# Kernel optimization log

Hardware: AMD Instinct MI355X
Metric: run time of the kernel (lower is better)

## Reference

```python
import jax, jax.numpy as jnp
import numpy as np

B, C, S = 16, 8, 128
DT, DX, DY = 0.001, 1.0, 1.0
NUM_STEPS = 10
EPS = 1e-6


def _thomas(a, b, c, d):
    """Batched Thomas tridiagonal solve. a,b,c,d: [M,N] rows; solve along N."""
    aT, bT, cT, dT = a.T, b.T, c.T, d.T  # [N, M]
    zero = jnp.zeros_like(dT[0])

    def fwd(carry, inp):
        cs_p, ds_p = carry
        ai, bi, ci, di = inp
        denom = bi - ai * cs_p + EPS  # i=0: cs_p=0 -> denom = b0 + eps (matches torch)
        cs = ci / denom
        ds = (di - ai * ds_p) / denom
        return (cs, ds), (cs, ds)

    _, (c_star, d_star) = jax.lax.scan(fwd, (zero, zero), (aT, bT, cT, dT))

    def bwd(x_next, inp):
        ci, di = inp
        x = di - ci * x_next
        return x, x

    _, xs = jax.lax.scan(bwd, d_star[-1], (c_star[:-1], d_star[:-1]), reverse=True)
    x = jnp.concatenate([xs, d_star[-1:]], axis=0)  # [N, M]
    return x.T


def _diffuse_rows(u2d, coeff):
    """Implicit 1D diffusion along last axis. u2d, coeff: [M,N]."""
    a = -coeff
    c = -coeff
    b = 1.0 + 2.0 * coeff
    b = b.at[:, 0].set(1.0 + coeff[:, 0])
    b = b.at[:, -1].set(1.0 + coeff[:, -1])
    return _thomas(a, b, c, u2d)


def _forward(u, alpha_base, beta_base, alpha_time_coeff, beta_time_coeff, channel_mixing):
    Bb, Cc, H, W = u.shape
    half = DT / 2.0
    t = 0.0
    for _ in range(NUM_STEPS):
        # x half-step (coefficient alpha at time t)
        alpha = jnp.clip(alpha_base + alpha_time_coeff * t, EPS, 10.0)
        u = jnp.einsum('dc,bchw->bdhw', channel_mixing, u)
        uf = u.reshape(Bb * Cc, H, W)
        af = jnp.broadcast_to(alpha[None], (Bb, Cc, H, W)).reshape(Bb * Cc, H, W)
        uf = _diffuse_rows(uf.reshape(-1, W), af.reshape(-1, W) * half / DX**2).reshape(Bb * Cc, H, W)
        t += half
        # y full step (coefficient beta at time t+dt/2)
        beta = jnp.clip(beta_base + beta_time_coeff * t, EPS, 10.0)
        bf = jnp.broadcast_to(beta[None], (Bb, Cc, H, W)).reshape(Bb * Cc, H, W)
        ut = uf.transpose(0, 2, 1).reshape(-1, H)
        bt = bf.transpose(0, 2, 1).reshape(-1, H)
        ut = _diffuse_rows(ut, bt * DT / DY**2)
        uf = ut.reshape(Bb * Cc, W, H).transpose(0, 2, 1)
        t += half
        # x half-step (coefficient alpha at time t+dt)
        alpha = jnp.clip(alpha_base + alpha_time_coeff * t, EPS, 10.0)
        af = jnp.broadcast_to(alpha[None], (Bb, Cc, H, W)).reshape(Bb * Cc, H, W)
        uf = _diffuse_rows(uf.reshape(-1, W), af.reshape(-1, W) * half / DX**2).reshape(Bb * Cc, H, W)
        u = uf.reshape(Bb, Cc, H, W)
    return u


def setup_inputs() -> dict:
    key = jax.random.key(0)
    k_u, k_cm, k_atc, k_btc = jax.random.split(key, 4)
    u = jax.random.normal(k_u, (B, C, S, S), dtype=jnp.float32)
    alpha_base = jnp.ones((C, S, S), dtype=jnp.float32)
    beta_base = jnp.ones((C, S, S), dtype=jnp.float32)
    alpha_time_coeff = jax.random.normal(k_atc, (C, S, S), dtype=jnp.float32) * 0.01
    beta_time_coeff = jax.random.normal(k_btc, (C, S, S), dtype=jnp.float32) * 0.01
    channel_mixing = jnp.eye(C, dtype=jnp.float32) + jax.random.normal(k_cm, (C, C), dtype=jnp.float32) * 0.01
    return {
        'u': u,
        'alpha_base': alpha_base,
        'beta_base': beta_base,
        'alpha_time_coeff': alpha_time_coeff,
        'beta_time_coeff': beta_time_coeff,
        'channel_mixing': channel_mixing,
    }


def reference(u, alpha_base, beta_base, alpha_time_coeff, beta_time_coeff, channel_mixing):
    return _forward(u, alpha_base, beta_base, alpha_time_coeff, beta_time_coeff, channel_mixing)
```

## Files before the change

### kernel.cpp

```cpp
#include <hip/hip_runtime.h>


constexpr int S_ = 128;
constexpr int RS = 129;
constexpr float EPSF = 1e-6f;

constexpr int OFF_X  = 0;
constexpr int OFF_C  = 32 * RS;
constexpr int OFF_B  = 64 * RS;
constexpr int OFF_HA = 96 * RS;

template <int N>
__device__ __forceinline__ void jrunN(const float (&e)[N], const float (&g)[N],
                                      float (&o)[N - 4]) {
    float x1[N];
    #pragma unroll
    for (int i = 1; i <= N - 2; ++i) x1[i] = fmaf(g[i], e[i - 1] + e[i + 1], e[i]);
    #pragma unroll
    for (int i = 2; i <= N - 3; ++i) o[i - 2] = fmaf(g[i], x1[i - 1] + x1[i + 1], e[i]);
}

template <bool HEAD, bool TAILMIX>
__global__ __launch_bounds__(512, 4) void step_kernel(
    const float* __restrict__ usrc, float* __restrict__ udst,
    const float* __restrict__ ab, const float* __restrict__ atc,
    const float* __restrict__ bbeta, const float* __restrict__ btc,
    const float* __restrict__ cm, float t_y, float t_x)
{
    constexpr int POOL = HEAD ? 160 * RS : 96 * RS;
    __shared__ float sP[POOL];
    const int tid = threadIdx.x;
    const int b   = blockIdx.x >> 5;
    const int h0  = (blockIdx.x & 31) << 2;

    if (HEAD) {
        #pragma unroll
        for (int m = 0; m < 2; ++m) {
            const int col = tid + 512 * m;
            const int c = col >> 7, w = col & 127;
            #pragma unroll
            for (int hh = 0; hh < 8; ++hh) {
                const int gh = h0 - 2 + hh;
                float v = 0.f;
                if (gh >= 0 && gh < S_) v = usrc[((b * 8 + c) * S_ + gh) * S_ + w];
                sP[(c * 8 + hh) * RS + w] = v;
            }
        }
        __syncthreads();
        {
            float M[64];
            #pragma unroll
            for (int i = 0; i < 64; ++i) M[i] = cm[i];
            #pragma unroll
            for (int m = 0; m < 2; ++m) {
                const int p = tid + 512 * m;
                const int hh = p >> 7, w = p & 127;
                float v[8], o[8];
                #pragma unroll
                for (int c = 0; c < 8; ++c) v[c] = sP[(c * 8 + hh) * RS + w];
                #pragma unroll
                for (int dd = 0; dd < 8; ++dd) {
                    float a = 0.f;
                    #pragma unroll
                    for (int c = 0; c < 8; ++c) a = fmaf(M[dd * 8 + c], v[c], a);
                    o[dd] = a;
                }
                #pragma unroll
                for (int c = 0; c < 8; ++c) sP[(c * 8 + hh) * RS + w] = o[c];
            }
        }
        __syncthreads();
        #pragma unroll
        for (int m = 0; m < 2; ++m) {
            const int run = tid + 512 * m;
            const int r64 = run & 63;
            const int wr  = run >> 6;
            const int c = r64 >> 3, hh = r64 & 7;
            const int gh = h0 - 2 + hh;
            const int w0 = wr * 8;
            const bool rowin = (gh >= 0 && gh < S_);
            float e[12], g[12];
            #pragma unroll
            for (int j = 0; j < 12; ++j) {
                const int wj = w0 - 2 + j;
                const bool win = (wj >= 0 && wj < S_);
                const float dv = win ? sP[r64 * RS + wj] : 0.f;
                float co = 0.f;
                if (rowin && win) {
                    float al = ab[(c * S_ + gh) * S_ + wj];
                    al = fminf(fmaxf(al, EPSF), 10.f);
                    co = al * 0.0005f;
                }
                const float nb = (wj == 0 || wj == S_ - 1) ? 1.f : 2.f;
                const float rb = __builtin_amdgcn_rcpf(fmaf(nb, co, 1.f) + EPSF);
                e[j] = rb * dv; g[j] = rb * co;
            }
            float o[8]; jrunN<12>(e, g, o);
            #pragma unroll
            for (int i = 0; i < 8; ++i) sP[OFF_HA + r64 * RS + w0 + i] = o[i];
        }
        __syncthreads();
    }

    #pragma unroll
    for (int m = 0; m < 2; ++m) {
        const int col = tid + 512 * m;
        const int c = col >> 7, w = col & 127;
        float e[8], g[8];
        #pragma unroll
        for (int hh = 0; hh < 8; ++hh) {
            const int gh = h0 - 2 + hh;
            const bool inr = (gh >= 0 && gh < S_);
            const int ghc = inr ? gh : 0;
            float dv;
            if (HEAD) dv = sP[OFF_HA + (c * 8 + hh) * RS + w];
            else      dv = inr ? usrc[((b * 8 + c) * S_ + ghc) * S_ + w] : 0.f;
            const int gc = (c * S_ + ghc) * S_ + w;
            float be = fmaf(btc[gc], t_y, bbeta[gc]);
            be = fminf(fmaxf(be, EPSF), 10.f);
            const float co = inr ? be * 0.001f : 0.f;
            const float nb = (gh == 0 || gh == S_ - 1) ? 1.f : 2.f;
            const float rb = __builtin_amdgcn_rcpf(fmaf(nb, co, 1.f) + EPSF);
            e[hh] = rb * dv; g[hh] = rb * co;
        }
        float o[4]; jrunN<8>(e, g, o);
        #pragma unroll
        for (int i = 0; i < 4; ++i) sP[OFF_X + (c * 4 + i) * RS + w] = o[i];
    }
    #pragma unroll
    for (int m = 0; m < 8; ++m) {
        const int p = tid + 512 * m;
        const int r = p >> 7, w = p & 127;
        const int c = r >> 2, ho = r & 3;
        const int gc = (c * S_ + h0 + ho) * S_ + w;
        float al = fmaf(atc[gc], t_x, ab[gc]);
        al = fminf(fmaxf(al, EPSF), 10.f);
        sP[OFF_C + r * RS + w] = al * 0.0005f;
    }
    __syncthreads();

    const int r32 = tid & 31, wr = tid >> 5;
    const int w0 = wr * 8;
    float rbk[12], gk[12], xo[8];
    {
        float e[12];
        #pragma unroll
        for (int j = 0; j < 12; ++j) {
            const int wj = w0 - 2 + j;
            const bool win = (wj >= 0 && wj < S_);
            const float co = win ? sP[OFF_C + r32 * RS + wj] : 0.f;
            const float dv = win ? sP[OFF_X + r32 * RS + wj] : 0.f;
            const float nb = (wj == 0 || wj == S_ - 1) ? 1.f : 2.f;
            const float rb = __builtin_amdgcn_rcpf(fmaf(nb, co, 1.f) + EPSF);
            rbk[j] = rb; gk[j] = rb * co;
            e[j] = rb * dv;
        }
        jrunN<12>(e, gk, xo);
    }

    if (TAILMIX) {
        #pragma unroll
        for (int i = 0; i < 8; ++i) sP[OFF_B + r32 * RS + w0 + i] = xo[i];
        __syncthreads();
        {
            float M[64];
            #pragma unroll
            for (int i = 0; i < 64; ++i) M[i] = cm[i];
            const int ho = tid >> 7, w = tid & 127;
            float v[8], o[8];
            #pragma unroll
            for (int c = 0; c < 8; ++c) v[c] = sP[OFF_B + (c * 4 + ho) * RS + w];
            #pragma unroll
            for (int dd = 0; dd < 8; ++dd) {
                float a = 0.f;
                #pragma unroll
                for (int c = 0; c < 8; ++c) a = fmaf(M[dd * 8 + c], v[c], a);
                o[dd] = a;
            }
            #pragma unroll
            for (int c = 0; c < 8; ++c) sP[OFF_X + (c * 4 + ho) * RS + w] = o[c];
        }
        __syncthreads();
        {
            const int c = r32 >> 2, ho = r32 & 3;
            float e[12];
            #pragma unroll
            for (int j = 0; j < 12; ++j) {
                const int wj = w0 - 2 + j;
                const bool win = (wj >= 0 && wj < S_);
                const float dv = win ? sP[OFF_X + r32 * RS + wj] : 0.f;
                e[j] = rbk[j] * dv;
            }
            float o[8]; jrunN<12>(e, gk, o);
            float4* dst4 = (float4*)&udst[((b * 8 + c) * S_ + h0 + ho) * S_ + w0];
            dst4[0] = make_float4(o[0], o[1], o[2], o[3]);
            dst4[1] = make_float4(o[4], o[5], o[6], o[7]);
        }
    } else {
        const int c = r32 >> 2, ho = r32 & 3;
        float4* dst4 = (float4*)&udst[((b * 8 + c) * S_ + h0 + ho) * S_ + w0];
        dst4[0] = make_float4(xo[0], xo[1], xo[2], xo[3]);
        dst4[1] = make_float4(xo[4], xo[5], xo[6], xo[7]);
    }
}

extern "C" void kernel_launch(void* const* d_in, const int* in_sizes, int n_in,
                              void* d_out, int out_size, void* d_ws, size_t ws_size,
                              hipStream_t stream) {
    const float* u_in = (const float*)d_in[0];
    const float* ab   = (const float*)d_in[1];
    const float* bbta = (const float*)d_in[2];
    const float* atc  = (const float*)d_in[3];
    const float* btc  = (const float*)d_in[4];
    const float* cm   = (const float*)d_in[5];
    float* uo = (float*)d_out;
    float* uw = (float*)d_ws;

    const dim3 g(512), blk(512);
    const float dt2 = 0.0005f;

    step_kernel<true, true><<<g, blk, 0, stream>>>(u_in, uw, ab, atc, bbta, btc, cm,
                                                   1 * dt2, 2 * dt2);
    const float* src = uw; float* dst = uo;
    for (int k = 1; k <= 8; ++k) {
        step_kernel<false, true><<<g, blk, 0, stream>>>(src, dst, ab, atc, bbta, btc, cm,
                                                        (2 * k + 1) * dt2, (2 * k + 2) * dt2);
        const float* ns = dst; dst = (dst == uo) ? uw : uo; src = ns;
    }
    step_kernel<false, false><<<g, blk, 0, stream>>>(src, dst, ab, atc, bbta, btc, cm,
                                                     19 * dt2, 20 * dt2);
}
```

Measured before the change: 188.0 us.

## Retile step kernel into 8-row by 64-column tiles with halo recompute

Each block now handles an 8-row by 64-column half-width tile (with a halo of 4 columns) instead of a full-width 4-row strip. The share of redundant halo rows in the y-direction truncated solve drops, while x-direction halos are recomputed per tile. Intermediate state moves into a padded 75-wide shared layout, and the mixing and x-sweep tail is restructured around it. The launch sequence now ping-pongs through two workspace buffers and writes the output only in the last launch. In exchange, the kernel does extra recomputation across the x halo and more guarded tail work with partially idle threads.

Result: slower. 222.6 us (+18.4%).

```diff
diff --git a/kernel.cpp b/kernel.cpp
--- a/kernel.cpp
+++ b/kernel.cpp
@@ -2,13 +2,12 @@
 
 
 constexpr int S_ = 128;
-constexpr int RS = 129;
 constexpr float EPSF = 1e-6f;
-
-constexpr int OFF_X  = 0;
-constexpr int OFF_C  = 32 * RS;
-constexpr int OFF_B  = 64 * RS;
-constexpr int OFF_HA = 96 * RS;
+constexpr int RSW = 75;
+constexpr int RST = 129;
+constexpr int OFF_A  = 0;
+constexpr int OFF_C  = 64 * RSW;
+constexpr int OFF_X0 = 96 * RST;
 
 template <int N>
 __device__ __forceinline__ void jrunN(const float (&e)[N], const float (&g)[N],
@@ -20,31 +19,32 @@
     for (int i = 2; i <= N - 3; ++i) o[i - 2] = fmaf(g[i], x1[i - 1] + x1[i + 1], e[i]);
 }
 
-template <bool HEAD, bool TAILMIX>
+template <bool HEAD, bool LASTK>
 __global__ __launch_bounds__(512, 4) void step_kernel(
     const float* __restrict__ usrc, float* __restrict__ udst,
     const float* __restrict__ ab, const float* __restrict__ atc,
     const float* __restrict__ bbeta, const float* __restrict__ btc,
     const float* __restrict__ cm, float t_y, float t_x)
 {
-    constexpr int POOL = HEAD ? 160 * RS : 96 * RS;
+    constexpr int POOL = HEAD ? (96 * RST + 96 * RSW) : (128 * RSW);
     __shared__ float sP[POOL];
-    const int tid = threadIdx.x;
-    const int b   = blockIdx.x >> 5;
-    const int h0  = (blockIdx.x & 31) << 2;
+    const int tid  = threadIdx.x;
+    const int rem  = blockIdx.x & 31;
+    const int b    = blockIdx.x >> 5;
+    const int h0   = (rem >> 1) << 3;
+    const int wh   = rem & 1;
+    const int woff = wh * 64 - 4;
 
     if (HEAD) {
         #pragma unroll
-        for (int m = 0; m < 2; ++m) {
-            const int col = tid + 512 * m;
-            const int c = col >> 7, w = col & 127;
-            #pragma unroll
-            for (int hh = 0; hh < 8; ++hh) {
-                const int gh = h0 - 2 + hh;
-                float v = 0.f;
-                if (gh >= 0 && gh < S_) v = usrc[((b * 8 + c) * S_ + gh) * S_ + w];
-                sP[(c * 8 + hh) * RS + w] = v;
-            }
+        for (int m = 0; m < 24; ++m) {
+            const int task = tid + 512 * m;
+            const int rr = task >> 7, w = task & 127;
+            const int c = rr / 12, hh = rr % 12;
+            const int gh = h0 - 2 + hh;
+            float v = 0.f;
+            if (gh >= 0 && gh < S_) v = usrc[((b * 8 + c) * S_ + gh) * S_ + w];
+            sP[rr * RST + w] = v;
         }
         __syncthreads();
         {
@@ -52,12 +52,12 @@
             #pragma unroll
             for (int i = 0; i < 64; ++i) M[i] = cm[i];
             #pragma unroll
-            for (int m = 0; m < 2; ++m) {
+            for (int m = 0; m < 3; ++m) {
                 const int p = tid + 512 * m;
                 const int hh = p >> 7, w = p & 127;
                 float v[8], o[8];
                 #pragma unroll
-                for (int c = 0; c < 8; ++c) v[c] = sP[(c * 8 + hh) * RS + w];
+                for (int c = 0; c < 8; ++c) v[c] = sP[(c * 12 + hh) * RST + w];
                 #pragma unroll
                 for (int dd = 0; dd < 8; ++dd) {
                     float a = 0.f;
@@ -66,30 +66,28 @@
                     o[dd] = a;
                 }
                 #pragma unroll
-                for (int c = 0; c < 8; ++c) sP[(c * 8 + hh) * RS + w] = o[c];
-            }
-        }
-        __syncthreads();
-        #pragma unroll
-        for (int m = 0; m < 2; ++m) {
-            const int run = tid + 512 * m;
-            const int r64 = run & 63;
-            const int wr  = run >> 6;
-            const int c = r64 >> 3, hh = r64 & 7;
+                for (int c = 0; c < 8; ++c) sP[(c * 12 + hh) * RST + w] = o[c];
+            }
+        }
+        __syncthreads();
+        #pragma unroll
+        for (int m = 0; m < 3; ++m) {
+            const int task = tid + 512 * m;
+            const int rr = task % 96, wr = task / 96;
+            const int c = rr / 12, hh = rr % 12;
             const int gh = h0 - 2 + hh;
+            const bool rowin = (gh >= 0 && gh < S_);
             const int w0 = wr * 8;
-            const bool rowin = (gh >= 0 && gh < S_);
             float e[12], g[12];
             #pragma unroll
             for (int j = 0; j < 12; ++j) {
                 const int wj = w0 - 2 + j;
                 const bool win = (wj >= 0 && wj < S_);
-                const float dv = win ? sP[r64 * RS + wj] : 0.f;
+                const float dv = win ? sP[rr * RST + wj] : 0.f;
                 float co = 0.f;
                 if (rowin && win) {
                     float al = ab[(c * S_ + gh) * S_ + wj];
-                    al = fminf(fmaxf(al, EPSF), 10.f);
-                    co = al * 0.0005f;
+                    co = fminf(fmaxf(al, EPSF), 10.f) * 0.0005f;
                 }
                 const float nb = (wj == 0 || wj == S_ - 1) ? 1.f : 2.f;
                 const float rb = __builtin_amdgcn_rcpf(fmaf(nb, co, 1.f) + EPSF);
@@ -97,110 +95,163 @@
             }
             float o[8]; jrunN<12>(e, g, o);
             #pragma unroll
-            for (int i = 0; i < 8; ++i) sP[OFF_HA + r64 * RS + w0 + i] = o[i];
+            for (int i = 0; i < 8; ++i) {
+                const int rel = w0 + i - woff;
+                if (rel >= 0 && rel < RSW) sP[OFF_X0 + rr * RSW + rel] = o[i];
+            }
         }
         __syncthreads();
     }
 
     #pragma unroll
     for (int m = 0; m < 2; ++m) {
-        const int col = tid + 512 * m;
-        const int c = col >> 7, w = col & 127;
-        float e[8], g[8];
-        #pragma unroll
-        for (int hh = 0; hh < 8; ++hh) {
-            const int gh = h0 - 2 + hh;
-            const bool inr = (gh >= 0 && gh < S_);
-            const int ghc = inr ? gh : 0;
-            float dv;
-            if (HEAD) dv = sP[OFF_HA + (c * 8 + hh) * RS + w];
-            else      dv = inr ? usrc[((b * 8 + c) * S_ + ghc) * S_ + w] : 0.f;
-            const int gc = (c * S_ + ghc) * S_ + w;
-            float be = fmaf(btc[gc], t_y, bbeta[gc]);
-            be = fminf(fmaxf(be, EPSF), 10.f);
-            const float co = inr ? be * 0.001f : 0.f;
-            const float nb = (gh == 0 || gh == S_ - 1) ? 1.f : 2.f;
+        const int task = tid + 512 * m;
+        if (task < 600) {
+            const int c = task / RSW, ws = task % RSW;
+            const int gw = woff + ws;
+            const bool wvalid = (gw >= 0 && gw < S_);
+            const int gwc = wvalid ? gw : 0;
+            float e[12], g[12];
+            #pragma unroll
+            for (int hh = 0; hh < 12; ++hh) {
+                const int gh = h0 - 2 + hh;
+                const bool inr = (gh >= 0 && gh < S_);
+                const int ghc = inr ? gh : 0;
+                float dv = 0.f;
+                if (inr && wvalid) {
+                    if (HEAD) dv = sP[OFF_X0 + (c * 12 + hh) * RSW + ws];
+                    else      dv = usrc[((b * 8 + c) * S_ + ghc) * S_ + gwc];
+                }
+                const int gc = (c * S_ + ghc) * S_ + gwc;
+                float be = fmaf(btc[gc], t_y, bbeta[gc]);
+                be = fminf(fmaxf(be, EPSF), 10.f);
+                const float co = inr ? be * 0.001f : 0.f;
+                const float nb = (gh == 0 || gh == S_ - 1) ? 1.f : 2.f;
+                const float rb = __builtin_amdgcn_rcpf(fmaf(nb, co, 1.f) + EPSF);
+                e[hh] = rb * dv; g[hh] = rb * co;
+            }
+            float o[8]; jrunN<12>(e, g, o);
+            #pragma unroll
+            for (int i = 0; i < 8; ++i) sP[OFF_A + (c * 8 + i) * RSW + ws] = o[i];
+        }
+    }
+    #pragma unroll
+    for (int m = 0; m < 10; ++m) {
+        const int task = tid + 512 * m;
+        if (task < 4800) {
+            const int r = task / RSW, wc = task % RSW;
+            const int gw = woff + wc;
+            float al = 0.f;
+            if (gw >= 0 && gw < S_) {
+                const int c = r >> 3, ho = r & 7;
+                const int gc = (c * S_ + h0 + ho) * S_ + gw;
+                al = fmaf(atc[gc], t_x, ab[gc]);
+                al = fminf(fmaxf(al, EPSF), 10.f) * 0.0005f;
+            }
+            sP[OFF_C + r * RSW + wc] = al;
+        }
+    }
+    __syncthreads();
+
+    if (LASTK) {
+        const int r = tid & 63, wr = tid >> 6;
+        const int c = r >> 3, ho = r & 7;
+        const int gw0 = wh * 64 + wr * 8;
+        float e[12], g[12];
+        #pragma unroll
+        for (int j = 0; j < 12; ++j) {
+            const int gj = gw0 - 2 + j;
+            const int aw = wr * 8 + 2 + j;
+            const bool win = (gj >= 0 && gj < S_);
+            const float co = win ? sP[OFF_C + r * RSW + aw] : 0.f;
+            const float dv = win ? sP[OFF_A + r * RSW + aw] : 0.f;
+            const float nb = (gj == 0 || gj == S_ - 1) ? 1.f : 2.f;
             const float rb = __builtin_amdgcn_rcpf(fmaf(nb, co, 1.f) + EPSF);
-            e[hh] = rb * dv; g[hh] = rb * co;
-        }
-        float o[4]; jrunN<8>(e, g, o);
-        #pragma unroll
-        for (int i = 0; i < 4; ++i) sP[OFF_X + (c * 4 + i) * RS + w] = o[i];
-    }
-    #pragma unroll
-    for (int m = 0; m < 8; ++m) {
-        const int p = tid + 512 * m;
-        const int r = p >> 7, w = p & 127;
-        const int c = r >> 2, ho = r & 3;
-        const int gc = (c * S_ + h0 + ho) * S_ + w;
-        float al = fmaf(atc[gc], t_x, ab[gc]);
-        al = fminf(fmaxf(al, EPSF), 10.f);
-        sP[OFF_C + r * RS + w] = al * 0.0005f;
-    }
-    __syncthreads();
-
-    const int r32 = tid & 31, wr = tid >> 5;
-    const int w0 = wr * 8;
-    float rbk[12], gk[12], xo[8];
-    {
-        float e[12];
-        #pragma unroll
-        for (int j = 0; j < 12; ++j) {
-            const int wj = w0 - 2 + j;
-            const bool win = (wj >= 0 && wj < S_);
-            const float co = win ? sP[OFF_C + r32 * RS + wj] : 0.f;
-            const float dv = win ? sP[OFF_X + r32 * RS + wj] : 0.f;
-            const float nb = (wj == 0 || wj == S_ - 1) ? 1.f : 2.f;
-            const float rb = __builtin_amdgcn_rcpf(fmaf(nb, co, 1.f) + EPSF);
-            rbk[j] = rb; gk[j] = rb * co;
-            e[j] = rb * dv;
-        }
-        jrunN<12>(e, gk, xo);
-    }
-
-    if (TAILMIX) {
-        #pragma unroll
-        for (int i = 0; i < 8; ++i) sP[OFF_B + r32 * RS + w0 + i] = xo[i];
+            e[j] = rb * dv; g[j] = rb * co;
+        }
+        float o[8]; jrunN<12>(e, g, o);
+        float4* dst4 = (float4*)&udst[((b * 8 + c) * S_ + h0 + ho) * S_ + gw0];
+        dst4[0] = make_float4(o[0], o[1], o[2], o[3]);
+        dst4[1] = make_float4(o[4], o[5], o[6], o[7]);
+    } else {
+        float xo[2][8];
+        #pragma unroll
+        for (int m = 0; m < 2; ++m) {
+            const int task = tid + 512 * m;
+            if (task < 576) {
+                const int r = task & 63, wr = task >> 6;
+                const int w0g = wh * 64 - 2 + wr * 8;
+                float e[12], g[12];
+                #pragma unroll
+                for (int j = 0; j < 12; ++j) {
+                    const int gj = w0g - 2 + j;
+                    const int aw = wr * 8 + j;
+                    const bool win = (gj >= 0 && gj < S_);
+                    const float co = win ? sP[OFF_C + r * RSW + aw] : 0.f;
+                    const float dv = win ? sP[OFF_A + r * RSW + aw] : 0.f;
+                    const float nb = (gj == 0 || gj == S_ - 1) ? 1.f : 2.f;
+                    const float rb = __builtin_amdgcn_rcpf(fmaf(nb, co, 1.f) + EPSF);
+                    e[j] = rb * dv; g[j] = rb * co;
+                }
+                jrunN<12>(e, g, xo[m]);
+            }
+        }
+        __syncthreads();
+        #pragma unroll
+        for (int m = 0; m < 2; ++m) {
+            const int task = tid + 512 * m;
+            if (task < 576) {
+                const int r = task & 63, wr = task >> 6;
+                #pragma unroll
+                for (int i = 0; i < 8; ++i)
+                    sP[OFF_A + r * RSW + wr * 8 + 2 + i] = xo[m][i];
+            }
+        }
         __syncthreads();
         {
             float M[64];
             #pragma unroll
             for (int i = 0; i < 64; ++i) M[i] = cm[i];
-            const int ho = tid >> 7, w = tid & 127;
-            float v[8], o[8];
-            #pragma unroll
-            for (int c = 0; c < 8; ++c) v[c] = sP[OFF_B + (c * 4 + ho) * RS + w];
-            #pragma unroll
-            for (int dd = 0; dd < 8; ++dd) {
-                float a = 0.f;
-                #pragma unroll
-                for (int c = 0; c < 8; ++c) a = fmaf(M[dd * 8 + c], v[c], a);
-                o[dd] = a;
-            }
-            #pragma unroll
-            for (int c = 0; c < 8; ++c) sP[OFF_X + (c * 4 + ho) * RS + w] = o[c];
-        }
-        __syncthreads();
-        {
-            const int c = r32 >> 2, ho = r32 & 3;
-            float e[12];
-            #pragma unroll
-            for (int j = 0; j < 12; ++j) {
-                const int wj = w0 - 2 + j;
-                const bool win = (wj >= 0 && wj < S_);
-                const float dv = win ? sP[OFF_X + r32 * RS + wj] : 0.f;
-                e[j] = rbk[j] * dv;
-            }
-            float o[8]; jrunN<12>(e, gk, o);
-            float4* dst4 = (float4*)&udst[((b * 8 + c) * S_ + h0 + ho) * S_ + w0];
-            dst4[0] = make_float4(o[0], o[1], o[2], o[3]);
-            dst4[1] = make_float4(o[4], o[5], o[6], o[7]);
-        }
-    } else {
-        const int c = r32 >> 2, ho = r32 & 3;
-        float4* dst4 = (float4*)&udst[((b * 8 + c) * S_ + h0 + ho) * S_ + w0];
-        dst4[0] = make_float4(xo[0], xo[1], xo[2], xo[3]);
-        dst4[1] = make_float4(xo[4], xo[5], xo[6], xo[7]);
+            #pragma unroll
+            for (int m = 0; m < 2; ++m) {
+                const int task = tid + 512 * m;
+                if (task < 600) {
+                    const int ho = task / RSW, aw = task % RSW;
+                    float v[8], o[8];
+                    #pragma unroll
+                    for (int c = 0; c < 8; ++c) v[c] = sP[OFF_A + (c * 8 + ho) * RSW + aw];
+                    #pragma unroll
+                    for (int dd = 0; dd < 8; ++dd) {
+                        float a = 0.f;
+                        #pragma unroll
+                        for (int c = 0; c < 8; ++c) a = fmaf(M[dd * 8 + c], v[c], a);
+                        o[dd] = a;
+                    }
+                    #pragma unroll
+                    for (int c = 0; c < 8; ++c) sP[OFF_A + (c * 8 + ho) * RSW + aw] = o[c];
+                }
+            }
+        }
+        __syncthreads();
+        const int r = tid & 63, wr = tid >> 6;
+        const int c = r >> 3, ho = r & 7;
+        const int gw0 = wh * 64 + wr * 8;
+        float e[12], g[12];
+        #pragma unroll
+        for (int j = 0; j < 12; ++j) {
+            const int gj = gw0 - 2 + j;
+            const int aw = wr * 8 + 2 + j;
+            const bool win = (gj >= 0 && gj < S_);
+            const float co = win ? sP[OFF_C + r * RSW + aw] : 0.f;
+            const float dv = win ? sP[OFF_A + r * RSW + aw] : 0.f;
+            const float nb = (gj == 0 || gj == S_ - 1) ? 1.f : 2.f;
+            const float rb = __builtin_amdgcn_rcpf(fmaf(nb, co, 1.f) + EPSF);
+            e[j] = rb * dv; g[j] = rb * co;
+        }
+        float o[8]; jrunN<12>(e, g, o);
+        float4* dst4 = (float4*)&udst[((b * 8 + c) * S_ + h0 + ho) * S_ + gw0];
+        dst4[0] = make_float4(o[0], o[1], o[2], o[3]);
+        dst4[1] = make_float4(o[4], o[5], o[6], o[7]);
     }
 }
 
@@ -213,20 +264,23 @@
     const float* atc  = (const float*)d_in[3];
     const float* btc  = (const float*)d_in[4];
     const float* cm   = (const float*)d_in[5];
-    float* uo = (float*)d_out;
-    float* uw = (float*)d_ws;
+    float* uo  = (float*)d_out;
+    float* uw1 = (float*)d_ws;
+    float* uw2 = (float*)d_ws + (16 * 8 * 128 * 128);
 
     const dim3 g(512), blk(512);
     const float dt2 = 0.0005f;
 
-    step_kernel<true, true><<<g, blk, 0, stream>>>(u_in, uw, ab, atc, bbta, btc, cm,
-                                                   1 * dt2, 2 * dt2);
-    const float* src = uw; float* dst = uo;
+    step_kernel<true, false><<<g, blk, 0, stream>>>(u_in, uw1, ab, atc, bbta, btc, cm,
+                                                    1 * dt2, 2 * dt2);
+    const float* s = uw1; float* d = uw2;
     for (int k = 1; k <= 8; ++k) {
-        step_kernel<false, true><<<g, blk, 0, stream>>>(src, dst, ab, atc, bbta, btc, cm,
-                                                        (2 * k + 1) * dt2, (2 * k + 2) * dt2);
-        const float* ns = dst; dst = (dst == uo) ? uw : uo; src = ns;
-    }
-    step_kernel<false, false><<<g, blk, 0, stream>>>(src, dst, ab, atc, bbta, btc, cm,
-                                                     19 * dt2, 20 * dt2);
+        step_kernel<false, false><<<g, blk, 0, stream>>>(s, d, ab, atc, bbta, btc, cm,
+                                                         (2 * k + 1) * dt2, (2 * k + 2) * dt2);
+        const float* ns = d;
+        d = (d == uw2) ? uw1 : uw2;
+        s = ns;
+    }
+    step_kernel<false, true><<<g, blk, 0, stream>>>(s, uo, ab, atc, bbta, btc, cm,
+                                                    19 * dt2, 20 * dt2);
 }
```
